# Performance work log

Hardware: AMD Instinct MI355X
Metric: run time of the kernel (lower is better)

Reference implementation:

```python
import jax, jax.numpy as jnp
import numpy as np


def setup_inputs() -> dict:
    key = jax.random.key(0)
    ks = jax.random.split(key, 7)
    B, T, inp_d, hid_d = 16, 4095, 2048, 2048
    scale = 0.02
    return {
        "x": jax.random.normal(ks[0], (B, inp_d), dtype=jnp.float32),
        "K_his": jax.random.normal(ks[1], (B, T, hid_d), dtype=jnp.float32),
        "V_his": jax.random.normal(ks[2], (B, T, hid_d), dtype=jnp.float32),
        "W_attn": jax.random.normal(ks[3], (inp_d, 3 * hid_d), dtype=jnp.float32) * scale,
        "b_attn": jax.random.normal(ks[4], (3 * hid_d,), dtype=jnp.float32) * scale,
        "W_proj": jax.random.normal(ks[5], (hid_d, hid_d), dtype=jnp.float32) * scale,
        "b_proj": jax.random.normal(ks[6], (hid_d,), dtype=jnp.float32) * scale,
        "n_head": 16,
    }


def reference(x, K_his, V_his, W_attn, b_attn, W_proj, b_proj, n_head):
    B = x.shape[0]
    qkv = x @ W_attn + b_attn                      # [B, 3*hid_d]
    q, k, v = jnp.split(qkv, 3, axis=-1)           # each [B, hid_d]
    hid_d = q.shape[-1]
    dh = hid_d // n_head
    # append current step to the KV cache
    K = jnp.concatenate([K_his, k[:, None, :]], axis=1)  # [B, T, hid_d]
    V = jnp.concatenate([V_his, v[:, None, :]], axis=1)
    T = K.shape[1]
    Kh = K.reshape(B, T, n_head, dh).transpose(0, 2, 1, 3)  # [B, H, T, dh]
    Vh = V.reshape(B, T, n_head, dh).transpose(0, 2, 1, 3)  # [B, H, T, dh]
    qh = q.reshape(B, n_head, dh, 1)                        # [B, H, dh, 1]
    scores = Kh @ qh                                        # [B, H, T, 1]
    # NOTE: faithful to the source: softmax over dim=-1 which has size 1 -> all ones
    att = jax.nn.softmax(scores, axis=-1)                   # [B, H, T, 1]
    v_next = jnp.swapaxes(Vh, -1, -2) @ att                 # [B, H, dh, 1]
    v_next = v_next.reshape(B, hid_d) @ W_proj + b_proj     # [B, hid_d]
    # faithful: reshape the head-major layout back to [B, T, hid_d]
    K_out = Kh.reshape(B, -1, hid_d)
    V_out = Vh.reshape(B, -1, hid_d)
    return K_out, V_out, v_next
```

## Files before the change

kernel.cpp:

```cpp
#include <hip/hip_runtime.h>


typedef float f4 __attribute__((ext_vector_type(4)));

__global__ void init_kernel(const float* __restrict__ b_attn,
                            const float* __restrict__ b_proj,
                            float* __restrict__ qkv,
                            float* __restrict__ colsum,
                            float* __restrict__ vnext) {
  int tid = blockIdx.x * blockDim.x + threadIdx.x;
  qkv[tid] = b_attn[2048 + (tid & 4095)];
  if (tid < 32768) {
    colsum[tid] = 0.0f;
    vnext[tid] = b_proj[tid & 2047];
  }
}

__global__ void small_gemm_atomic(const float* __restrict__ X,
                                  const float* __restrict__ W,
                                  int ldw, int col0,
                                  float* __restrict__ out, int ncols) {
  int j  = blockIdx.x * 512 + threadIdx.x * 2;
  int k0 = blockIdx.y * 64;
  const float* wp = W + (size_t)k0 * ldw + col0 + j;
  float2 acc[16];
#pragma unroll
  for (int b = 0; b < 16; ++b) acc[b] = make_float2(0.f, 0.f);
  for (int kk = 0; kk < 64; ++kk) {
    float2 w = *(const float2*)(wp + (size_t)kk * ldw);
    const float* xp = X + k0 + kk;
#pragma unroll
    for (int b = 0; b < 16; ++b) {
      float xv = xp[(size_t)b * 2048];
      acc[b].x = fmaf(xv, w.x, acc[b].x);
      acc[b].y = fmaf(xv, w.y, acc[b].y);
    }
  }
#pragma unroll
  for (int b = 0; b < 16; ++b) {
    atomicAdd(&out[b * ncols + j],     acc[b].x);
    atomicAdd(&out[b * ncols + j + 1], acc[b].y);
  }
}

__global__ void __launch_bounds__(256, 4)
copy_transpose(const float* __restrict__ K_his,
               const float* __restrict__ V_his,
               const float* __restrict__ qkv,
               float* __restrict__ out,
               float* __restrict__ colsum) {
  const int b     = blockIdx.y;
  const int which = blockIdx.z;
  const int gx    = blockIdx.x;
  const int tid   = threadIdx.x;
  const int tbase = gx * 128;

  const float* src  = which ? V_his : K_his;
  const float* srcb = src + (size_t)b * 8386560ull;
  const float* qsrc = qkv + b * 4096 + which * 2048;
  float* outb = out + ((size_t)which << 27) + ((size_t)b << 23);

  __shared__ float lds[8192];

  f4 acc0 = {0.f, 0.f, 0.f, 0.f};
  f4 acc1 = {0.f, 0.f, 0.f, 0.f};
  const int c0 = tid * 4;
  const int c1 = 1024 + tid * 4;

  const int o    = (tid & 127) * 4;
  const int s_l  = o >> 7;
  const int d    = o & 127;
  const int hsel = tid >> 7;

  for (int p = 0; p < 32; ++p) {
    f4 v[8];
#pragma unroll
    for (int j = 0; j < 8; ++j) {
      const int r = j >> 1;
      const int c = (j & 1) ? c1 : c0;
      const int t = tbase + p * 4 + r;
      const float* pr = (t == 4095) ? qsrc : (srcb + (size_t)t * 2048u);
      v[j] = __builtin_nontemporal_load((const f4*)(pr + c));
    }
#pragma unroll
    for (int j = 0; j < 8; ++j)
      *(f4*)(&lds[(j * 256 + tid) * 4]) = v[j];
    if (which) {
#pragma unroll
      for (int j = 0; j < 8; j += 2) { acc0 += v[j]; acc1 += v[j + 1]; }
    }
    __syncthreads();

    const int tgrp = gx * 8 + (p >> 2);
    const int obase = (p & 3) * 512;
    f4 w[8];
#pragma unroll
    for (int pass = 0; pass < 8; ++pass) {
      const int h = pass * 2 + hsel;
      w[pass] = *(const f4*)(&lds[s_l * 2048 + h * 128 + d]);
    }
#pragma unroll
    for (int pass = 0; pass < 8; ++pass) {
      const int h = pass * 2 + hsel;
      float* op = outb + (size_t)(h * 256 + tgrp) * 2048u + (unsigned)(obase + o);
      __builtin_nontemporal_store(w[pass], (f4*)op);
    }
    __syncthreads();
  }

  if (which) {
    float* cp = colsum + b * 2048;
    atomicAdd(cp + c0 + 0, acc0.x);
    atomicAdd(cp + c0 + 1, acc0.y);
    atomicAdd(cp + c0 + 2, acc0.z);
    atomicAdd(cp + c0 + 3, acc0.w);
    atomicAdd(cp + c1 + 0, acc1.x);
    atomicAdd(cp + c1 + 1, acc1.y);
    atomicAdd(cp + c1 + 2, acc1.z);
    atomicAdd(cp + c1 + 3, acc1.w);
  }
}

extern "C" void kernel_launch(void* const* d_in, const int* in_sizes, int n_in,
                              void* d_out, int out_size, void* d_ws, size_t ws_size,
                              hipStream_t stream) {
  const float* x      = (const float*)d_in[0];
  const float* K_his  = (const float*)d_in[1];
  const float* V_his  = (const float*)d_in[2];
  const float* W_attn = (const float*)d_in[3];
  const float* b_attn = (const float*)d_in[4];
  const float* W_proj = (const float*)d_in[5];
  const float* b_proj = (const float*)d_in[6];

  float* out    = (float*)d_out;
  float* qkv    = (float*)d_ws;
  float* colsum = qkv + 16 * 4096;
  float* vnext  = out + 268435456ull;

  init_kernel<<<256, 256, 0, stream>>>(b_attn, b_proj, qkv, colsum, vnext);
  small_gemm_atomic<<<dim3(8, 32), 256, 0, stream>>>(x, W_attn, 6144, 2048, qkv, 4096);
  copy_transpose<<<dim3(32, 16, 2), 256, 0, stream>>>(K_his, V_his, qkv, out, colsum);
  small_gemm_atomic<<<dim3(4, 32), 256, 0, stream>>>(colsum, W_proj, 2048, 0, vnext, 2048);
}
```

Baseline: 482.4 us.

## Transpose KV cache directly from registers without LDS staging, finer grid

The copy-transpose kernel no longer stages tiles in shared memory with two barriers per step. Each wave now loads row segments whose layout lets it write them straight to the head-major output positions from registers. Column sums for V are accumulated per thread, combined across half-waves with shuffles and across waves through LDS once at the end. The grid grows fourfold with fewer rows per block, and the launch bound is relaxed to allow more registers. The cost is heavier register use for 16 accumulator vectors, which may reduce occupancy.

```diff
diff --git a/kernel.cpp b/kernel.cpp
--- a/kernel.cpp
+++ b/kernel.cpp
@@ -43,7 +43,7 @@
   }
 }
 
-__global__ void __launch_bounds__(256, 4)
+__global__ void __launch_bounds__(256, 2)
 copy_transpose(const float* __restrict__ K_his,
                const float* __restrict__ V_his,
                const float* __restrict__ qkv,
@@ -53,7 +53,10 @@
   const int which = blockIdx.z;
   const int gx    = blockIdx.x;
   const int tid   = threadIdx.x;
-  const int tbase = gx * 128;
+  const int l     = tid & 63;
+  const int w     = tid >> 6;
+  const int off   = 4 * (l & 31);
+  const bool hi   = (l >= 32);
 
   const float* src  = which ? V_his : K_his;
   const float* srcb = src + (size_t)b * 8386560ull;
@@ -62,62 +65,72 @@
 
   __shared__ float lds[8192];
 
-  f4 acc0 = {0.f, 0.f, 0.f, 0.f};
-  f4 acc1 = {0.f, 0.f, 0.f, 0.f};
-  const int c0 = tid * 4;
-  const int c1 = 1024 + tid * 4;
+  f4 accA[8], accB[8];
+#pragma unroll
+  for (int i = 0; i < 8; ++i) {
+    accA[i] = (f4){0.f, 0.f, 0.f, 0.f};
+    accB[i] = (f4){0.f, 0.f, 0.f, 0.f};
+  }
 
-  const int o    = (tid & 127) * 4;
-  const int s_l  = o >> 7;
-  const int d    = o & 127;
-  const int hsel = tid >> 7;
+  for (int gsub = 0; gsub < 2; ++gsub) {
+    const int g = gx * 2 + gsub;
+#pragma unroll
+    for (int it = 0; it < 2; ++it) {
+      const int rp = it * 4 + w;
+      const int t0 = g * 16 + rp * 2;
+      const float* r0 = srcb + (size_t)t0 * 2048u;
+      const float* r1 = (t0 + 1 == 4095) ? qsrc : (r0 + 2048);
+      const float* rowp = hi ? r1 : r0;
 
-  for (int p = 0; p < 32; ++p) {
-    f4 v[8];
+      f4 sa[8], sb[8];
 #pragma unroll
-    for (int j = 0; j < 8; ++j) {
-      const int r = j >> 1;
-      const int c = (j & 1) ? c1 : c0;
-      const int t = tbase + p * 4 + r;
-      const float* pr = (t == 4095) ? qsrc : (srcb + (size_t)t * 2048u);
-      v[j] = __builtin_nontemporal_load((const f4*)(pr + c));
+      for (int i = 0; i < 8; ++i) {
+        sa[i] = __builtin_nontemporal_load((const f4*)(rowp + i * 256 + off));
+        sb[i] = __builtin_nontemporal_load((const f4*)(rowp + i * 256 + 128 + off));
+      }
+      if (which) {
+#pragma unroll
+        for (int i = 0; i < 8; ++i) { accA[i] += sa[i]; accB[i] += sb[i]; }
+      }
+#pragma unroll
+      for (int i = 0; i < 8; ++i) {
+        float* o0 = outb + (size_t)(2 * i * 256 + g) * 2048u + (unsigned)(rp * 256 + 4 * l);
+        __builtin_nontemporal_store(sa[i], (f4*)o0);
+        __builtin_nontemporal_store(sb[i], (f4*)(o0 + 256 * 2048));
+      }
     }
-#pragma unroll
-    for (int j = 0; j < 8; ++j)
-      *(f4*)(&lds[(j * 256 + tid) * 4]) = v[j];
-    if (which) {
-#pragma unroll
-      for (int j = 0; j < 8; j += 2) { acc0 += v[j]; acc1 += v[j + 1]; }
-    }
-    __syncthreads();
-
-    const int tgrp = gx * 8 + (p >> 2);
-    const int obase = (p & 3) * 512;
-    f4 w[8];
-#pragma unroll
-    for (int pass = 0; pass < 8; ++pass) {
-      const int h = pass * 2 + hsel;
-      w[pass] = *(const f4*)(&lds[s_l * 2048 + h * 128 + d]);
-    }
-#pragma unroll
-    for (int pass = 0; pass < 8; ++pass) {
-      const int h = pass * 2 + hsel;
-      float* op = outb + (size_t)(h * 256 + tgrp) * 2048u + (unsigned)(obase + o);
-      __builtin_nontemporal_store(w[pass], (f4*)op);
-    }
-    __syncthreads();
   }
 
   if (which) {
-    float* cp = colsum + b * 2048;
-    atomicAdd(cp + c0 + 0, acc0.x);
-    atomicAdd(cp + c0 + 1, acc0.y);
-    atomicAdd(cp + c0 + 2, acc0.z);
-    atomicAdd(cp + c0 + 3, acc0.w);
-    atomicAdd(cp + c1 + 0, acc1.x);
-    atomicAdd(cp + c1 + 1, acc1.y);
-    atomicAdd(cp + c1 + 2, acc1.z);
-    atomicAdd(cp + c1 + 3, acc1.w);
+#pragma unroll
+    for (int i = 0; i < 8; ++i) {
+      accA[i].x += __shfl_xor(accA[i].x, 32);
+      accA[i].y += __shfl_xor(accA[i].y, 32);
+      accA[i].z += __shfl_xor(accA[i].z, 32);
+      accA[i].w += __shfl_xor(accA[i].w, 32);
+      accB[i].x += __shfl_xor(accB[i].x, 32);
+      accB[i].y += __shfl_xor(accB[i].y, 32);
+      accB[i].z += __shfl_xor(accB[i].z, 32);
+      accB[i].w += __shfl_xor(accB[i].w, 32);
+    }
+    if (l < 32) {
+#pragma unroll
+      for (int i = 0; i < 8; ++i) {
+        *(f4*)(&lds[w * 2048 + i * 256 + off])       = accA[i];
+        *(f4*)(&lds[w * 2048 + i * 256 + 128 + off]) = accB[i];
+      }
+    }
+    __syncthreads();
+    const int c = tid * 8;
+    f4 s0 = *(const f4*)(&lds[c]) + *(const f4*)(&lds[2048 + c])
+          + *(const f4*)(&lds[4096 + c]) + *(const f4*)(&lds[6144 + c]);
+    f4 s1 = *(const f4*)(&lds[c + 4]) + *(const f4*)(&lds[2048 + c + 4])
+          + *(const f4*)(&lds[4096 + c + 4]) + *(const f4*)(&lds[6144 + c + 4]);
+    float* cp = colsum + b * 2048 + c;
+    atomicAdd(cp + 0, s0.x); atomicAdd(cp + 1, s0.y);
+    atomicAdd(cp + 2, s0.z); atomicAdd(cp + 3, s0.w);
+    atomicAdd(cp + 4, s1.x); atomicAdd(cp + 5, s1.y);
+    atomicAdd(cp + 6, s1.z); atomicAdd(cp + 7, s1.w);
   }
 }
 
@@ -139,6 +152,6 @@
 
   init_kernel<<<256, 256, 0, stream>>>(b_attn, b_proj, qkv, colsum, vnext);
   small_gemm_atomic<<<dim3(8, 32), 256, 0, stream>>>(x, W_attn, 6144, 2048, qkv, 4096);
-  copy_transpose<<<dim3(32, 16, 2), 256, 0, stream>>>(K_his, V_his, qkv, out, colsum);
+  copy_transpose<<<dim3(128, 16, 2), 256, 0, stream>>>(K_his, V_his, qkv, out, colsum);
   small_gemm_atomic<<<dim3(4, 32), 256, 0, stream>>>(colsum, W_proj, 2048, 0, vnext, 2048);
 }
```

After: 488.8 us. Within noise of the previous version (+1.3%).
